# Kernel optimization log

Hardware: AMD Instinct MI355X
Metric: run time of the kernel (lower is better)

## Reference

```python
import jax, jax.numpy as jnp
import numpy as np

# static graph structure: B graphs, each with NPER nodes and DEG*NPER edges
B = 128        # graphs in batch
NPER = 400     # nodes per graph (fMRI atlas ROIs)
DEG = 16       # avg degree
EPG = NPER * DEG
E = B * EPG    # 819200 edges total
F_IN = 400     # num_features
H = 128        # hidden dim of GraphConv
C = 2          # num_classes
K1, K2, K3 = 320, 256, 205  # ceil(0.8*400), ceil(0.8*320), ceil(0.8*256)


def setup_inputs() -> dict:
    key = jax.random.key(0)
    ks = jax.random.split(key, 24)
    x = jax.random.normal(ks[0], (B * NPER, F_IN), dtype=jnp.float32)
    # edges constrained within each graph (PyG batched disjoint-union convention)
    src_l = jax.random.randint(ks[1], (B, EPG), 0, NPER)
    dst_l = jax.random.randint(ks[2], (B, EPG), 0, NPER)
    off = (jnp.arange(B, dtype=jnp.int32) * NPER)[:, None]
    edge_src = (src_l + off).reshape(-1).astype(jnp.int32)
    edge_dst = (dst_l + off).reshape(-1).astype(jnp.int32)
    batch = jnp.repeat(jnp.arange(B, dtype=jnp.int32), NPER)
    s = 0.05
    p = {
        'Wrel1': jax.random.normal(ks[3], (H, F_IN)) * s,
        'Wroot1': jax.random.normal(ks[4], (H, F_IN)) * s,
        'b1': jnp.zeros((H,), jnp.float32),
        'pw1': jax.random.normal(ks[5], (H,)) * s,
        'Wrel2': jax.random.normal(ks[6], (H, H)) * s,
        'Wroot2': jax.random.normal(ks[7], (H, H)) * s,
        'b2': jnp.zeros((H,), jnp.float32),
        'pw2': jax.random.normal(ks[8], (H,)) * s,
        'Wrel3': jax.random.normal(ks[9], (H, H)) * s,
        'Wroot3': jax.random.normal(ks[10], (H, H)) * s,
        'b3': jnp.zeros((H,), jnp.float32),
        'pw3': jax.random.normal(ks[11], (H,)) * s,
        'W1': jax.random.normal(ks[12], (128, 256)) * s,
        'bl1': jnp.zeros((128,), jnp.float32),
        'W2': jax.random.normal(ks[13], (64, 128)) * s,
        'bl2': jnp.zeros((64,), jnp.float32),
        'W3': jax.random.normal(ks[14], (C, 64)) * s,
        'bl3': jnp.zeros((C,), jnp.float32),
    }
    return dict(x=x, edge_src=edge_src, edge_dst=edge_dst, batch=batch, **p)


def _graph_conv(x, src, dst, emask, Wrel, b, Wroot):
    # PyG GraphConv: lin_rel(sum_j x_j) + lin_root(x_i); masked edges contribute 0
    msg = x[src] * emask[:, None]
    agg = jax.ops.segment_sum(msg, dst, num_segments=x.shape[0])
    return agg @ Wrel.T + b + x @ Wroot.T


def _topk_pool(x, src, dst, emask, w, npg, k):
    # score = x.w / ||w||; keep top-k per graph; gate kept x by tanh(score)
    score = (x @ w) / (jnp.linalg.norm(w) + 1e-16)
    vals, idx = jax.lax.top_k(score.reshape(B, npg), k)      # [B,k]
    perm = (jnp.arange(B, dtype=jnp.int32)[:, None] * npg + idx).reshape(-1)
    xk = x[perm] * jnp.tanh(vals).reshape(-1)[:, None]
    new_id = jnp.full((B * npg,), -1, jnp.int32).at[perm].set(
        jnp.arange(B * k, dtype=jnp.int32))
    ns, nd = new_id[src], new_id[dst]
    keep = (ns >= 0) & (nd >= 0)
    em2 = emask * keep.astype(emask.dtype)
    return xk, jnp.where(keep, ns, 0), jnp.where(keep, nd, 0), em2


def _readout(x, k):
    xr = x.reshape(B, k, H)
    return jnp.concatenate([xr.max(axis=1), xr.mean(axis=1)], axis=1)  # [B,256]


def reference(x, edge_src, edge_dst, batch,
              Wrel1, Wroot1, b1, pw1, Wrel2, Wroot2, b2, pw2,
              Wrel3, Wroot3, b3, pw3, W1, bl1, W2, bl2, W3, bl3):
    em = jnp.ones((E,), jnp.float32)
    h = jax.nn.relu(_graph_conv(x, edge_src, edge_dst, em, Wrel1, b1, Wroot1))
    h, s, d, em = _topk_pool(h, edge_src, edge_dst, em, pw1, NPER, K1)
    x1 = _readout(h, K1)
    h = jax.nn.relu(_graph_conv(h, s, d, em, Wrel2, b2, Wroot2))
    h, s, d, em = _topk_pool(h, s, d, em, pw2, K1, K2)
    x2 = _readout(h, K2)
    h = jax.nn.relu(_graph_conv(h, s, d, em, Wrel3, b3, Wroot3))
    h, s, d, em = _topk_pool(h, s, d, em, pw3, K2, K3)
    x3 = _readout(h, K3)
    z = x1 + x2 + x3
    z = jax.nn.relu(z @ W1.T + bl1)  # dropout is identity in eval mode
    z = jax.nn.relu(z @ W2.T + bl2)
    return jax.nn.log_softmax(z @ W3.T + bl3, axis=-1)
```

## Files before the change

### kernel.cpp

```cpp
#include <hip/hip_runtime.h>
#include <math.h>

#define BATCH 128
#define NPER 400
#define EPG 6400
#define NEDGE 819200
#define F_IN 400
#define HD 128
#define K1 320
#define K2 256
#define K3 205

typedef __bf16 bf16x8 __attribute__((ext_vector_type(8)));
typedef float f32x4 __attribute__((ext_vector_type(4)));

__device__ __forceinline__ unsigned short f2bf(float f) {
    unsigned u = __builtin_bit_cast(unsigned, f);
    unsigned r = u + 0x7fffu + ((u >> 16) & 1u);
    return (unsigned short)(r >> 16);
}
__device__ __forceinline__ float bf2f(unsigned short s) {
    unsigned u = ((unsigned)s) << 16;
    return __builtin_bit_cast(float, u);
}

static constexpr size_t SZ_TREL = 51200ull * 128 * 4;
static constexpr size_t OFF_TREL = 0;
static constexpr size_t OFF_H    = OFF_TREL + SZ_TREL;
static constexpr size_t OFF_HP   = OFF_H + SZ_TREL;
static constexpr size_t OFF_SC   = OFF_HP + 40960ull * 128 * 4;
static constexpr size_t OFF_ES   = OFF_SC + 51200ull * 4;
static constexpr size_t OFF_ED   = OFF_ES + (size_t)NEDGE * 4;
static constexpr size_t OFF_EM   = OFF_ED + (size_t)NEDGE * 4;
static constexpr size_t OFF_Z    = OFF_EM + (size_t)NEDGE * 4;
static constexpr size_t OFF_COFF = OFF_Z + 128ull * 256 * 4;
static constexpr size_t OFF_CDEG = OFF_COFF + 51200ull * 4;
static constexpr size_t OFF_CSRC = OFF_CDEG + 51200ull * 4;
static constexpr size_t OFF_W1H  = OFF_CSRC + (size_t)NEDGE * 4;
static constexpr size_t OFF_W1L  = OFF_W1H + 16ull * 13 * 512 * 2;
static constexpr size_t OFF_W2H  = OFF_W1L + 16ull * 13 * 512 * 2;
static constexpr size_t OFF_W2L  = OFF_W2H + 16ull * 4 * 512 * 2;
static constexpr size_t OFF_W3H  = OFF_W2L + 16ull * 4 * 512 * 2;
static constexpr size_t OFF_W3L  = OFF_W3H + 16ull * 4 * 512 * 2;

__global__ __launch_bounds__(64) void prep_w_all(
    const float* __restrict__ Wrel1, const float* __restrict__ Wroot1,
    const float* __restrict__ Wrel2, const float* __restrict__ Wroot2,
    const float* __restrict__ Wrel3, const float* __restrict__ Wroot3,
    unsigned short* __restrict__ b1h, unsigned short* __restrict__ b1l,
    unsigned short* __restrict__ b2h, unsigned short* __restrict__ b2l,
    unsigned short* __restrict__ b3h, unsigned short* __restrict__ b3l) {
    const int layer = blockIdx.z;
    const int s = blockIdx.x;
    const int ntile = blockIdx.y;
    const int Ks = (layer == 0) ? 13 : 4;
    const int Kd = (layer == 0) ? F_IN : HD;
    if (s >= Ks) return;
    const float* Wrel  = (layer == 0) ? Wrel1  : (layer == 1) ? Wrel2  : Wrel3;
    const float* Wroot = (layer == 0) ? Wroot1 : (layer == 1) ? Wroot2 : Wroot3;
    unsigned short* bh = (layer == 0) ? b1h : (layer == 1) ? b2h : b3h;
    unsigned short* bl = (layer == 0) ? b1l : (layer == 1) ? b2l : b3l;
    const int t = threadIdx.x;
    const int rowin = t & 15, qd = t >> 4;
    const int n = ntile * 16 + rowin;
    const int k = s * 32 + qd * 8;
    const float* src = (n < 128) ? &Wrel[(n & 127) * Kd] : &Wroot[(n & 127) * Kd];
    unsigned short hv[8], lv[8];
#pragma unroll
    for (int e = 0; e < 8; e++) {
        float f = (k + e < Kd) ? src[k + e] : 0.f;
        unsigned short hi = f2bf(f);
        hv[e] = hi;
        lv[e] = f2bf(f - bf2f(hi));
    }
    size_t o = ((size_t)ntile * Ks + s) * 512 + (size_t)t * 8;
#pragma unroll
    for (int e = 0; e < 8; e++) { bh[o + e] = hv[e]; bl[o + e] = lv[e]; }
}

template <int Ks, int Kd>
__global__ __launch_bounds__(256) void gemm_mfma(
    const float* __restrict__ A,
    const unsigned short* __restrict__ bh_p, const unsigned short* __restrict__ bl_p,
    float* __restrict__ t_rel, float* __restrict__ h) {
    const int tid = threadIdx.x;
    const int lane = tid & 63;
    const int wv = tid >> 6;
    const int lm = lane & 15;
    const int qd = (lane >> 4) & 3;
    const int m0 = blockIdx.x * 64;
    const int nt0 = wv * 4;

    f32x4 acc[4][4];
#pragma unroll
    for (int i = 0; i < 4; i++)
#pragma unroll
        for (int j = 0; j < 4; j++) acc[i][j] = (f32x4){0.f, 0.f, 0.f, 0.f};

    const float* Abase = A + (size_t)(m0 + lm) * Kd + qd * 8;

#pragma unroll
    for (int s = 0; s < Ks; s++) {
        bf16x8 ah[4], al[4];
#pragma unroll
        for (int i = 0; i < 4; i++) {
            float4 f0, f1;
            if (s * 32 + qd * 8 < Kd) {
                const float* p = Abase + (size_t)i * 16 * Kd + s * 32;
                f0 = *(const float4*)p;
                f1 = *(const float4*)(p + 4);
            } else {
                f0 = make_float4(0.f, 0.f, 0.f, 0.f);
                f1 = f0;
            }
            float fe[8] = {f0.x, f0.y, f0.z, f0.w, f1.x, f1.y, f1.z, f1.w};
#pragma unroll
            for (int e = 0; e < 8; e++) {
                __bf16 hb = (__bf16)fe[e];
                ah[i][e] = hb;
                al[i][e] = (__bf16)(fe[e] - (float)hb);
            }
        }
        bf16x8 bh[4], bl[4];
#pragma unroll
        for (int j = 0; j < 4; j++)
            bh[j] = *(const bf16x8*)&bh_p[((size_t)(nt0 + j) * Ks + s) * 512 + lane * 8];
#pragma unroll
        for (int j = 0; j < 4; j++)
            bl[j] = *(const bf16x8*)&bl_p[((size_t)(nt0 + j) * Ks + s) * 512 + lane * 8];
#pragma unroll
        for (int j = 0; j < 4; j++)
#pragma unroll
            for (int i = 0; i < 4; i++)
                acc[i][j] = __builtin_amdgcn_mfma_f32_16x16x32_bf16(
                    ah[i], bh[j], acc[i][j], 0, 0, 0);
#pragma unroll
        for (int j = 0; j < 4; j++)
#pragma unroll
            for (int i = 0; i < 4; i++)
                acc[i][j] = __builtin_amdgcn_mfma_f32_16x16x32_bf16(
                    al[i], bh[j], acc[i][j], 0, 0, 0);
#pragma unroll
        for (int j = 0; j < 4; j++)
#pragma unroll
            for (int i = 0; i < 4; i++)
                acc[i][j] = __builtin_amdgcn_mfma_f32_16x16x32_bf16(
                    ah[i], bl[j], acc[i][j], 0, 0, 0);
    }
    float* out = (wv < 2) ? t_rel : h;
    const int colbase = (wv & 1) * 64;
#pragma unroll
    for (int i = 0; i < 4; i++)
#pragma unroll
        for (int j = 0; j < 4; j++) {
            int row = m0 + i * 16 + qd * 4;
            int col = colbase + j * 16 + lm;
#pragma unroll
            for (int r = 0; r < 4; r++)
                out[(size_t)(row + r) * 128 + col] = acc[i][j][r];
        }
}

__global__ __launch_bounds__(1024) void csr_build0(
    const int* __restrict__ gsrc, const int* __restrict__ gdst,
    int* __restrict__ csr_off, int* __restrict__ csr_deg, int* __restrict__ csr_src) {
    __shared__ int cnt[NPER];
    __shared__ int cur[NPER];
    __shared__ int sscan[512];
    const int g = blockIdx.x;
    const int t = threadIdx.x;
    for (int i = t; i < NPER; i += 1024) cnt[i] = 0;
    __syncthreads();
    for (int e = t; e < EPG; e += 1024) {
        int dl = gdst[g * EPG + e] - g * NPER;
        atomicAdd(&cnt[dl], 1);
    }
    __syncthreads();
    if (t < 512) sscan[t] = (t < NPER) ? cnt[t] : 0;
    __syncthreads();
    for (int d = 1; d < 512; d <<= 1) {
        int v = 0;
        if (t < 512 && t >= d) v = sscan[t - d];
        __syncthreads();
        if (t < 512 && t >= d) sscan[t] += v;
        __syncthreads();
    }
    if (t < NPER) {
        int excl = (t == 0) ? 0 : sscan[t - 1];
        int st = g * EPG + excl;
        csr_off[g * NPER + t] = st;
        csr_deg[g * NPER + t] = cnt[t];
        cur[t] = st;
    }
    __syncthreads();
    for (int e = t; e < EPG; e += 1024) {
        int eg = g * EPG + e;
        int dl = gdst[eg] - g * NPER;
        int slot = atomicAdd(&cur[dl], 1);
        csr_src[slot] = gsrc[eg];
    }
}

__global__ __launch_bounds__(256) void agg_score(
    const float* __restrict__ t_rel,
    const int* __restrict__ csr_off, const int* __restrict__ csr_deg,
    const int* __restrict__ csr_src,
    const float* __restrict__ bias, const float* __restrict__ pw,
    float* __restrict__ h, float* __restrict__ sc, int npg) {
    const int xcd = blockIdx.x & 7;
    const int j = blockIdx.x >> 3;
    const int bpg = npg >> 2;
    const int graph = xcd * (BATCH / 8) + j / bpg;
    const int nblk = j - (j / bpg) * bpg;
    const int wid = graph * npg + nblk * 4 + (threadIdx.x >> 6);
    const int lane = threadIdx.x & 63;

    const int start = csr_off[wid];
    const int deg = csr_deg[wid];
    const size_t fo = (size_t)lane * 2;
    float a0 = 0.f, a1 = 0.f, b0 = 0.f, b1 = 0.f;
    float c0 = 0.f, c1 = 0.f, d0 = 0.f, d1 = 0.f;
    int e = 0;
    for (; e + 4 <= deg; e += 4) {
        int s0 = csr_src[start + e];
        int s1 = csr_src[start + e + 1];
        int s2 = csr_src[start + e + 2];
        int s3 = csr_src[start + e + 3];
        float2 v0 = *(const float2*)&t_rel[(size_t)s0 * 128 + fo];
        float2 v1 = *(const float2*)&t_rel[(size_t)s1 * 128 + fo];
        float2 v2 = *(const float2*)&t_rel[(size_t)s2 * 128 + fo];
        float2 v3 = *(const float2*)&t_rel[(size_t)s3 * 128 + fo];
        a0 += v0.x; a1 += v0.y;
        b0 += v1.x; b1 += v1.y;
        c0 += v2.x; c1 += v2.y;
        d0 += v3.x; d1 += v3.y;
    }
    for (; e < deg; e++) {
        int s0 = csr_src[start + e];
        float2 v0 = *(const float2*)&t_rel[(size_t)s0 * 128 + fo];
        a0 += v0.x; a1 += v0.y;
    }
    a0 += b0 + c0 + d0;
    a1 += b1 + c1 + d1;

    float2 bb = *(const float2*)&bias[fo];
    size_t o = (size_t)wid * 128 + fo;
    float2 hv = *(const float2*)&h[o];
    hv.x = fmaxf(hv.x + a0 + bb.x, 0.f);
    hv.y = fmaxf(hv.y + a1 + bb.y, 0.f);
    *(float2*)&h[o] = hv;
    float2 pp = *(const float2*)&pw[fo];
    float d = hv.x * pp.x + hv.y * pp.y;
    float nr = pp.x * pp.x + pp.y * pp.y;
#pragma unroll
    for (int off = 32; off; off >>= 1) {
        d += __shfl_down(d, off, 64);
        nr += __shfl_down(nr, off, 64);
    }
    if (lane == 0) sc[wid] = d / (sqrtf(nr) + 1e-16f);
}

__device__ __forceinline__ bool rank_before(float as, int ai, float bs, int bi) {
    return (as > bs) || (as == bs && ai < bi);
}
__global__ __launch_bounds__(1024) void topk_pool(
    const float* __restrict__ sc, const float* __restrict__ h,
    float* __restrict__ hp, float* __restrict__ z,
    const int* __restrict__ gsrc, const int* __restrict__ gdst,
    int* __restrict__ es, int* __restrict__ ed, int* __restrict__ em,
    int* __restrict__ csr_off, int* __restrict__ csr_deg, int* __restrict__ csr_src,
    int npg, int k, int mode) {
    __shared__ float sk[512];
    __shared__ int si[512];
    __shared__ int nid[NPER];
    __shared__ float tgs[K1];
    __shared__ int packed[EPG];
    __shared__ int cnt[K1];
    __shared__ int cur[K1];
    __shared__ int sscan[512];
    __shared__ float pmx[8][128], psm[8][128];
    const int g = blockIdx.x;
    const int t = threadIdx.x;

    if (t < 512) {
        sk[t] = (t < npg) ? sc[g * npg + t] : -INFINITY;
        si[t] = t;
    }
    __syncthreads();
    for (int size = 2; size <= 512; size <<= 1) {
        for (int stride = size >> 1; stride; stride >>= 1) {
            if (t < 512) {
                int i = t, j = i ^ stride;
                if (j > i) {
                    bool up = ((i & size) == 0);
                    float a = sk[i], b = sk[j];
                    int ai = si[i], bi = si[j];
                    bool doswap = up ? rank_before(b, bi, a, ai)
                                     : rank_before(a, ai, b, bi);
                    if (doswap) { sk[i] = b; sk[j] = a; si[i] = bi; si[j] = ai; }
                }
            }
            __syncthreads();
        }
    }
    if (t < 512) {
        int orig = si[t];
        if (orig < npg) nid[orig] = (t < k) ? t : -1;
        if (t < k) tgs[t] = tanhf(sk[t]);
    }
    if (t < K1) cnt[t] = 0;
    __syncthreads();

    {
        const int f = t & 127;
        const int jq = t >> 7;
        float mx = -INFINITY, sm = 0.f;
        for (int j = jq; j < k; j += 8) {
            float v = h[(size_t)(g * npg + si[j]) * 128 + f] * tgs[j];
            if (mode != 2) hp[(size_t)(g * k + j) * 128 + f] = v;
            mx = fmaxf(mx, v);
            sm += v;
        }
        pmx[jq][f] = mx; psm[jq][f] = sm;
        __syncthreads();
        if (t < 128) {
            mx = pmx[0][t]; sm = psm[0][t];
#pragma unroll
            for (int q = 1; q < 8; q++) {
                mx = fmaxf(mx, pmx[q][t]);
                sm += psm[q][t];
            }
            z[g * 256 + t] += mx;
            z[g * 256 + 128 + t] += sm / (float)k;
        }
    }
    if (mode == 2) return;

    for (int e = t; e < EPG; e += 1024) {
        int eg = g * EPG + e;
        int sl, dl, m;
        if (mode == 0) { sl = gsrc[eg] - g * NPER; dl = gdst[eg] - g * NPER; m = 1; }
        else           { sl = es[eg]; dl = ed[eg]; m = em[eg]; }
        int ns = nid[sl], nd = nid[dl];
        int keep = (m && ns >= 0 && nd >= 0) ? 1 : 0;
        es[eg] = keep ? ns : 0;
        ed[eg] = keep ? nd : 0;
        em[eg] = keep;
        packed[e] = keep ? (ns | (nd << 16)) : -1;
        if (keep) atomicAdd(&cnt[nd], 1);
    }
    __syncthreads();
    if (t < 512) sscan[t] = (t < k) ? cnt[t] : 0;
    __syncthreads();
    for (int d = 1; d < 512; d <<= 1) {
        int v = 0;
        if (t < 512 && t >= d) v = sscan[t - d];
        __syncthreads();
        if (t < 512 && t >= d) sscan[t] += v;
        __syncthreads();
    }
    if (t < k) {
        int excl = (t == 0) ? 0 : sscan[t - 1];
        int st = g * EPG + excl;
        csr_off[g * k + t] = st;
        csr_deg[g * k + t] = cnt[t];
        cur[t] = st;
    }
    __syncthreads();
    for (int e = t; e < EPG; e += 1024) {
        int p = packed[e];
        if (p >= 0) {
            int ns = p & 0xffff, nd = p >> 16;
            int slot = atomicAdd(&cur[nd], 1);
            csr_src[slot] = g * k + ns;
        }
    }
}

__global__ __launch_bounds__(256) void mlp_head(const float* __restrict__ z,
                                                const float* __restrict__ W1,
                                                const float* __restrict__ bl1,
                                                const float* __restrict__ W2,
                                                const float* __restrict__ bl2,
                                                const float* __restrict__ W3,
                                                const float* __restrict__ bl3,
                                                float* __restrict__ out) {
    __shared__ float zs[256], l1[128], l2[64];
    const int g = blockIdx.x, t = threadIdx.x;
    zs[t] = z[g * 256 + t];
    __syncthreads();
    if (t < 128) {
        float s = bl1[t];
        const float* w = &W1[t * 256];
        for (int i = 0; i < 256; i++) s += w[i] * zs[i];
        l1[t] = fmaxf(s, 0.f);
    }
    __syncthreads();
    if (t < 64) {
        float s = bl2[t];
        const float* w = &W2[t * 128];
        for (int i = 0; i < 128; i++) s += w[i] * l1[i];
        l2[t] = fmaxf(s, 0.f);
    }
    __syncthreads();
    if (t == 0) {
        float a = bl3[0], b = bl3[1];
        for (int i = 0; i < 64; i++) { a += W3[i] * l2[i]; b += W3[64 + i] * l2[i]; }
        float m = fmaxf(a, b);
        float lse = m + logf(expf(a - m) + expf(b - m));
        out[g * 2 + 0] = a - lse;
        out[g * 2 + 1] = b - lse;
    }
}

extern "C" void kernel_launch(void* const* d_in, const int* in_sizes, int n_in,
                              void* d_out, int out_size, void* d_ws, size_t ws_size,
                              hipStream_t stream) {
    const float* x        = (const float*)d_in[0];
    const int*   edge_src = (const int*)d_in[1];
    const int*   edge_dst = (const int*)d_in[2];
    const float* Wrel1 = (const float*)d_in[4];
    const float* Wroot1= (const float*)d_in[5];
    const float* b1    = (const float*)d_in[6];
    const float* pw1   = (const float*)d_in[7];
    const float* Wrel2 = (const float*)d_in[8];
    const float* Wroot2= (const float*)d_in[9];
    const float* b2    = (const float*)d_in[10];
    const float* pw2   = (const float*)d_in[11];
    const float* Wrel3 = (const float*)d_in[12];
    const float* Wroot3= (const float*)d_in[13];
    const float* b3    = (const float*)d_in[14];
    const float* pw3   = (const float*)d_in[15];
    const float* W1    = (const float*)d_in[16];
    const float* bl1   = (const float*)d_in[17];
    const float* W2    = (const float*)d_in[18];
    const float* bl2   = (const float*)d_in[19];
    const float* W3    = (const float*)d_in[20];
    const float* bl3   = (const float*)d_in[21];

    char* ws = (char*)d_ws;
    float* t_rel = (float*)(ws + OFF_TREL);
    float* h     = (float*)(ws + OFF_H);
    float* hp    = (float*)(ws + OFF_HP);
    float* sc    = (float*)(ws + OFF_SC);
    int*   es    = (int*)(ws + OFF_ES);
    int*   ed    = (int*)(ws + OFF_ED);
    int*   em    = (int*)(ws + OFF_EM);
    float* z     = (float*)(ws + OFF_Z);
    int*   coff  = (int*)(ws + OFF_COFF);
    int*   cdeg  = (int*)(ws + OFF_CDEG);
    int*   csrc  = (int*)(ws + OFF_CSRC);
    unsigned short* w1h = (unsigned short*)(ws + OFF_W1H);
    unsigned short* w1l = (unsigned short*)(ws + OFF_W1L);
    unsigned short* w2h = (unsigned short*)(ws + OFF_W2H);
    unsigned short* w2l = (unsigned short*)(ws + OFF_W2L);
    unsigned short* w3h = (unsigned short*)(ws + OFF_W3H);
    unsigned short* w3l = (unsigned short*)(ws + OFF_W3L);

    hipMemsetAsync(z, 0, 128ull * 256 * 4, stream);
    prep_w_all<<<dim3(13, 16, 3), 64, 0, stream>>>(
        Wrel1, Wroot1, Wrel2, Wroot2, Wrel3, Wroot3,
        w1h, w1l, w2h, w2l, w3h, w3l);
    csr_build0<<<BATCH, 1024, 0, stream>>>(edge_src, edge_dst, coff, cdeg, csrc);

    gemm_mfma<13, F_IN><<<800, 256, 0, stream>>>(x, w1h, w1l, t_rel, h);
    agg_score<<<51200 / 4, 256, 0, stream>>>(t_rel, coff, cdeg, csrc, b1, pw1,
                                             h, sc, NPER);
    topk_pool<<<BATCH, 1024, 0, stream>>>(sc, h, hp, z, edge_src, edge_dst,
                                          es, ed, em, coff, cdeg, csrc,
                                          NPER, K1, 0);

    gemm_mfma<4, HD><<<640, 256, 0, stream>>>(hp, w2h, w2l, t_rel, h);
    agg_score<<<40960 / 4, 256, 0, stream>>>(t_rel, coff, cdeg, csrc, b2, pw2,
                                             h, sc, K1);
    topk_pool<<<BATCH, 1024, 0, stream>>>(sc, h, hp, z, nullptr, nullptr,
                                          es, ed, em, coff, cdeg, csrc,
                                          K1, K2, 1);

    gemm_mfma<4, HD><<<512, 256, 0, stream>>>(hp, w3h, w3l, t_rel, h);
    agg_score<<<32768 / 4, 256, 0, stream>>>(t_rel, coff, cdeg, csrc, b3, pw3,
                                             h, sc, K2);
    topk_pool<<<BATCH, 1024, 0, stream>>>(sc, h, nullptr, z, nullptr, nullptr,
                                          es, ed, em, coff, cdeg, csrc,
                                          K2, K3, 2);

    mlp_head<<<BATCH, 256, 0, stream>>>(z, W1, bl1, W2, bl2, W3, bl3, (float*)d_out);
}
```

Measured before the change: 472.6 us.

## Stage A tiles into swizzled LDS with async double-buffered global loads

The GEMM now stages the fp32 A tile for each K step into a double-buffered LDS array using global_load_lds async copies, with an XOR swizzle to avoid bank conflicts. The next step's load is issued before the current step's MFMAs run. Previously each wave read A directly from global memory, and all four waves read the same rows redundantly. This shares A across waves and overlaps load latency with compute, at the cost of a barrier per K step and clamped out-of-range addresses.

After: 464.4 us. About the same (-1.8%).

```diff
diff --git a/kernel.cpp b/kernel.cpp
--- a/kernel.cpp
+++ b/kernel.cpp
@@ -22,6 +22,12 @@
 __device__ __forceinline__ float bf2f(unsigned short s) {
     unsigned u = ((unsigned)s) << 16;
     return __builtin_bit_cast(float, u);
+}
+
+__device__ __forceinline__ void async_ld16(const void* g, void* lds) {
+    __builtin_amdgcn_global_load_lds(
+        (const __attribute__((address_space(1))) unsigned int*)g,
+        (__attribute__((address_space(3))) unsigned int*)lds, 16, 0, 0);
 }
 
 static constexpr size_t SZ_TREL = 51200ull * 128 * 4;
@@ -83,6 +89,7 @@
     const float* __restrict__ A,
     const unsigned short* __restrict__ bh_p, const unsigned short* __restrict__ bl_p,
     float* __restrict__ t_rel, float* __restrict__ h) {
+    __shared__ float Alds[2][2048];
     const int tid = threadIdx.x;
     const int lane = tid & 63;
     const int wv = tid >> 6;
@@ -91,24 +98,47 @@
     const int m0 = blockIdx.x * 64;
     const int nt0 = wv * 4;
 
+    const int srow = wv * 8 + (lane >> 3);
+    const int sgr  = (lane & 7) ^ (lane >> 3);
+    const size_t amax = (size_t)gridDim.x * 64 * Kd * 4 - 16;
+    const char* Abyte = (const char*)A;
+
+    const int ga = (((2 * qd)     ^ (lm & 7)) << 4);
+    const int gb = (((2 * qd + 1) ^ (lm & 7)) << 4);
+
     f32x4 acc[4][4];
 #pragma unroll
     for (int i = 0; i < 4; i++)
 #pragma unroll
         for (int j = 0; j < 4; j++) acc[i][j] = (f32x4){0.f, 0.f, 0.f, 0.f};
 
-    const float* Abase = A + (size_t)(m0 + lm) * Kd + qd * 8;
-
-#pragma unroll
-    for (int s = 0; s < Ks; s++) {
+    auto stage = [&](int buf, int s) {
+#pragma unroll
+        for (int p = 0; p < 2; ++p) {
+            const int row = srow + p * 32;
+            size_t go = (size_t)(m0 + row) * Kd * 4 + (size_t)s * 128
+                        + ((size_t)sgr << 4);
+            if (go > amax) go = amax;
+            async_ld16(Abyte + go, &Alds[buf][p * 1024 + wv * 256]);
+        }
+    };
+
+    stage(0, 0);
+    __syncthreads();
+
+#pragma unroll
+    for (int s = 0; s < Ks; ++s) {
+        if (s + 1 < Ks) stage((s + 1) & 1, s + 1);
+
+        const char* Ab = (const char*)&Alds[s & 1][0];
         bf16x8 ah[4], al[4];
 #pragma unroll
         for (int i = 0; i < 4; i++) {
             float4 f0, f1;
             if (s * 32 + qd * 8 < Kd) {
-                const float* p = Abase + (size_t)i * 16 * Kd + s * 32;
-                f0 = *(const float4*)p;
-                f1 = *(const float4*)(p + 4);
+                const char* base = Ab + (lm + i * 16) * 128;
+                f0 = *(const float4*)(base + ga);
+                f1 = *(const float4*)(base + gb);
             } else {
                 f0 = make_float4(0.f, 0.f, 0.f, 0.f);
                 f1 = f0;
@@ -146,6 +176,8 @@
             for (int i = 0; i < 4; i++)
                 acc[i][j] = __builtin_amdgcn_mfma_f32_16x16x32_bf16(
                     ah[i], bl[j], acc[i][j], 0, 0, 0);
+
+        __syncthreads();
     }
     float* out = (wv < 2) ? t_rel : h;
     const int colbase = (wv & 1) * 64;
```

## Stage A tiles through double-buffered LDS with register prefetch in MFMA GEMM

Applied to the files above, without the earlier changes.

Before this change, every wave loaded and split the full 64-row A tile from global memory on its own, so the four waves repeated the same loads and bf16 hi/lo conversions. Now each thread loads one row slice, converts it once, and writes it into a double-buffered LDS tile, prefetching two stages ahead in registers. The MFMA block runs at raised wave priority, and a barrier after each stage keeps the buffers in sync. Launch bounds now request 3 blocks per SIMD. The change adds 16KB of LDS and one barrier per k-step, and the occupancy hint may cause register spills.

Result: faster. 444.2 us (-6.0%).

```diff
diff --git a/kernel.cpp b/kernel.cpp
--- a/kernel.cpp
+++ b/kernel.cpp
@@ -79,10 +79,11 @@
 }
 
 template <int Ks, int Kd>
-__global__ __launch_bounds__(256) void gemm_mfma(
+__global__ __launch_bounds__(256, 3) void gemm_mfma(
     const float* __restrict__ A,
     const unsigned short* __restrict__ bh_p, const unsigned short* __restrict__ bl_p,
     float* __restrict__ t_rel, float* __restrict__ h) {
+    __shared__ char Alds[2][8192];
     const int tid = threadIdx.x;
     const int lane = tid & 63;
     const int wv = tid >> 6;
@@ -91,61 +92,99 @@
     const int m0 = blockIdx.x * 64;
     const int nt0 = wv * 4;
 
+    const int srow = tid >> 2;
+    const int sqd = tid & 3;
+    const int woff = ((srow >> 4) << 10) + (sqd << 8) + ((srow & 15) << 4);
+    const float* Arow = A + (size_t)(m0 + srow) * Kd + sqd * 8;
+
     f32x4 acc[4][4];
 #pragma unroll
     for (int i = 0; i < 4; i++)
 #pragma unroll
         for (int j = 0; j < 4; j++) acc[i][j] = (f32x4){0.f, 0.f, 0.f, 0.f};
 
-    const float* Abase = A + (size_t)(m0 + lm) * Kd + qd * 8;
-
-#pragma unroll
-    for (int s = 0; s < Ks; s++) {
+    auto gload = [&](int s, float4& x0, float4& x1) {
+        if (s * 32 + sqd * 8 < Kd) {
+            const float* p = Arow + s * 32;
+            x0 = *(const float4*)p;
+            x1 = *(const float4*)(p + 4);
+        } else {
+            x0 = make_float4(0.f, 0.f, 0.f, 0.f);
+            x1 = x0;
+        }
+    };
+    auto cvwrite = [&](int buf, const float4& x0, const float4& x1) {
+        float fe[8] = {x0.x, x0.y, x0.z, x0.w, x1.x, x1.y, x1.z, x1.w};
+        bf16x8 hv, lv;
+#pragma unroll
+        for (int e = 0; e < 8; e++) {
+            __bf16 hb = (__bf16)fe[e];
+            hv[e] = hb;
+            lv[e] = (__bf16)(fe[e] - (float)hb);
+        }
+        *(bf16x8*)(&Alds[buf][woff]) = hv;
+        *(bf16x8*)(&Alds[buf][4096 + woff]) = lv;
+    };
+
+    float4 r0a, r0b, r1a, r1b;
+    gload(0, r0a, r0b);
+    if (Ks > 1) gload(1, r1a, r1b);
+    cvwrite(0, r0a, r0b);
+    asm volatile("s_waitcnt lgkmcnt(0)" ::: "memory");
+    __builtin_amdgcn_s_barrier();
+    asm volatile("" ::: "memory");
+
+#pragma unroll
+    for (int s = 0; s < Ks; ++s) {
+        bf16x8 bhc[4], blc[4];
+#pragma unroll
+        for (int j = 0; j < 4; j++)
+            bhc[j] = *(const bf16x8*)&bh_p[((size_t)(nt0 + j) * Ks + s) * 512 + lane * 8];
+#pragma unroll
+        for (int j = 0; j < 4; j++)
+            blc[j] = *(const bf16x8*)&bl_p[((size_t)(nt0 + j) * Ks + s) * 512 + lane * 8];
+
+        const char* Ab = &Alds[s & 1][0];
         bf16x8 ah[4], al[4];
 #pragma unroll
         for (int i = 0; i < 4; i++) {
-            float4 f0, f1;
-            if (s * 32 + qd * 8 < Kd) {
-                const float* p = Abase + (size_t)i * 16 * Kd + s * 32;
-                f0 = *(const float4*)p;
-                f1 = *(const float4*)(p + 4);
-            } else {
-                f0 = make_float4(0.f, 0.f, 0.f, 0.f);
-                f1 = f0;
-            }
-            float fe[8] = {f0.x, f0.y, f0.z, f0.w, f1.x, f1.y, f1.z, f1.w};
-#pragma unroll
-            for (int e = 0; e < 8; e++) {
-                __bf16 hb = (__bf16)fe[e];
-                ah[i][e] = hb;
-                al[i][e] = (__bf16)(fe[e] - (float)hb);
-            }
-        }
-        bf16x8 bh[4], bl[4];
-#pragma unroll
-        for (int j = 0; j < 4; j++)
-            bh[j] = *(const bf16x8*)&bh_p[((size_t)(nt0 + j) * Ks + s) * 512 + lane * 8];
-#pragma unroll
-        for (int j = 0; j < 4; j++)
-            bl[j] = *(const bf16x8*)&bl_p[((size_t)(nt0 + j) * Ks + s) * 512 + lane * 8];
+            ah[i] = *(const bf16x8*)(Ab + i * 1024 + lane * 16);
+            al[i] = *(const bf16x8*)(Ab + 4096 + i * 1024 + lane * 16);
+        }
+
+        if (s + 1 < Ks) {
+            if ((s + 1) & 1) cvwrite((s + 1) & 1, r1a, r1b);
+            else             cvwrite((s + 1) & 1, r0a, r0b);
+        }
+        if (s + 2 < Ks) {
+            if ((s + 2) & 1) gload(s + 2, r1a, r1b);
+            else             gload(s + 2, r0a, r0b);
+        }
+
+        __builtin_amdgcn_s_setprio(1);
 #pragma unroll
         for (int j = 0; j < 4; j++)
 #pragma unroll
             for (int i = 0; i < 4; i++)
                 acc[i][j] = __builtin_amdgcn_mfma_f32_16x16x32_bf16(
-                    ah[i], bh[j], acc[i][j], 0, 0, 0);
+                    ah[i], bhc[j], acc[i][j], 0, 0, 0);
 #pragma unroll
         for (int j = 0; j < 4; j++)
 #pragma unroll
             for (int i = 0; i < 4; i++)
                 acc[i][j] = __builtin_amdgcn_mfma_f32_16x16x32_bf16(
-                    al[i], bh[j], acc[i][j], 0, 0, 0);
+                    al[i], bhc[j], acc[i][j], 0, 0, 0);
 #pragma unroll
         for (int j = 0; j < 4; j++)
 #pragma unroll
             for (int i = 0; i < 4; i++)
                 acc[i][j] = __builtin_amdgcn_mfma_f32_16x16x32_bf16(
-                    ah[i], bl[j], acc[i][j], 0, 0, 0);
+                    ah[i], blc[j], acc[i][j], 0, 0, 0);
+        __builtin_amdgcn_s_setprio(0);
+
+        asm volatile("s_waitcnt lgkmcnt(0)" ::: "memory");
+        __builtin_amdgcn_s_barrier();
+        asm volatile("" ::: "memory");
     }
     float* out = (wv < 2) ? t_rel : h;
     const int colbase = (wv & 1) * 64;
```
